# Performance work log

Hardware: AMD Instinct MI355X
Metric: run time of the kernel (lower is better)

## Reference

```python
import jax, jax.numpy as jnp
import numpy as np

DIM = 768
NUM_HEADS = 12
HEAD_DIM = DIM // NUM_HEADS
SCALE = HEAD_DIM ** -0.5


def setup_inputs() -> dict:
    key = jax.random.key(0)
    ks = jax.random.split(key, 4)
    x = jax.random.normal(ks[0], (8, 1024, DIM), dtype=jnp.float32)
    # nn.Linear stores weight as [out, in]; we keep that convention.
    w_qkv = jax.random.normal(ks[1], (3 * DIM, DIM), dtype=jnp.float32) * (DIM ** -0.5)
    w_proj = jax.random.normal(ks[2], (DIM, DIM), dtype=jnp.float32) * (DIM ** -0.5)
    b_proj = jax.random.normal(ks[3], (DIM,), dtype=jnp.float32) * 0.02
    return {"x": x, "w_qkv": w_qkv, "w_proj": w_proj, "b_proj": b_proj}


def reference(x, w_qkv, w_proj, b_proj):
    B, N, C = x.shape
    H, D = NUM_HEADS, HEAD_DIM
    # qkv: [B, N, 3C] -> [3, B, H, N, D]
    qkv = jnp.einsum('bnc,oc->bno', x, w_qkv)
    qkv = qkv.reshape(B, N, 3, H, D).transpose(2, 0, 3, 1, 4)
    q, k, v = qkv[0] * SCALE, qkv[1], qkv[2]
    # attention scores [B, H, N, N]
    attn = jnp.einsum('bhnd,bhmd->bhnm', q, k)
    attn = jax.nn.softmax(attn, axis=-1)
    # weighted values -> [B, N, C]
    out = jnp.einsum('bhnm,bhmd->bhnd', attn, v)
    out = out.transpose(0, 2, 1, 3).reshape(B, N, C)
    # output projection
    return jnp.einsum('bnc,oc->bno', out, w_proj) + b_proj
```

## Files before the change

### kernel.cpp

```cpp
#include <hip/hip_runtime.h>
#include <hip/hip_bf16.h>
#include <math.h>


typedef unsigned short u16;
typedef __attribute__((ext_vector_type(8))) short bf16x8;
typedef __attribute__((ext_vector_type(4))) float f32x4;
typedef __attribute__((ext_vector_type(4))) unsigned int u32x4;

#define MFMA_BF16(a, b, c) __builtin_amdgcn_mfma_f32_16x16x32_bf16((a), (b), (c), 0, 0, 0)

static __device__ __forceinline__ void gld_lds16(const void* g, void* l) {
  __builtin_amdgcn_global_load_lds(
      (__attribute__((address_space(1))) void*)(g),
      (__attribute__((address_space(3))) void*)(l), 16, 0, 0);
}

static __device__ __forceinline__ u16 f2bf(float f) {
  __hip_bfloat16 h = __float2bfloat16(f);
  return *(u16*)&h;
}

static __device__ __forceinline__ float fast_exp2(float x) {
#if __has_builtin(__builtin_amdgcn_exp2f)
  return __builtin_amdgcn_exp2f(x);
#else
  return exp2f(x);
#endif
}

static __device__ __forceinline__ void conv4(const float* src, u16* dst, int i) {
  const float4 v = *(const float4*)(src + i);
  float f0 = v.x, f1 = v.y, f2 = v.z, f3 = v.w;
  if (!isfinite(f0)) f0 = 0.f;
  if (!isfinite(f1)) f1 = 0.f;
  if (!isfinite(f2)) f2 = 0.f;
  if (!isfinite(f3)) f3 = 0.f;
  ushort4 o;
  o.x = f2bf(f0); o.y = f2bf(f1); o.z = f2bf(f2); o.w = f2bf(f3);
  *(ushort4*)(dst + i) = o;
}

__global__ __launch_bounds__(256) void convert3_kernel(
    const float* __restrict__ x,  u16* __restrict__ xb,
    const float* __restrict__ wq, u16* __restrict__ wqb,
    const float* __restrict__ wp, u16* __restrict__ wpb)
{
  const int blk = blockIdx.x;
  if (blk < 6144)      conv4(x,  xb,  (blk * 256 + threadIdx.x) * 4);
  else if (blk < 7872) conv4(wq, wqb, ((blk - 6144) * 256 + threadIdx.x) * 4);
  else                 conv4(wp, wpb, ((blk - 7872) * 256 + threadIdx.x) * 4);
}

__device__ __forceinline__ void gemm_tile_768(
    const u16* __restrict__ A, const u16* __restrict__ B,
    int m0, int n0, u16* ldsA, u16* ldsB, f32x4 acc[4][4])
{
  const int tid  = threadIdx.x;
  const int lane = tid & 63;
  const int wave = tid >> 6;
  const int quad = lane >> 4;
  const int l16  = lane & 15;
  const int wm = wave >> 1, wn = wave & 1;

  const u16* gA[4]; const u16* gB[4]; int ldsoff[4];
#pragma unroll
  for (int it = 0; it < 4; ++it) {
    const int c   = it * 256 + tid;
    const int row = c >> 3;
    const int cc  = (c & 7) ^ (row & 7);
    gA[it] = A + (size_t)(m0 + row) * 768 + cc * 8;
    gB[it] = B + (size_t)(n0 + row) * 768 + cc * 8;
    ldsoff[it] = (it * 256 + wave * 64) * 8;
  }

  for (int kt = 0; kt < 12; ++kt) {
    __syncthreads();
#pragma unroll
    for (int it = 0; it < 4; ++it) {
      gld_lds16(gA[it] + kt * 64, ldsA + ldsoff[it]);
      gld_lds16(gB[it] + kt * 64, ldsB + ldsoff[it]);
    }
    __syncthreads();
#pragma unroll
    for (int kc = 0; kc < 2; ++kc) {
      bf16x8 av[4], bv[4];
#pragma unroll
      for (int i = 0; i < 4; ++i) {
        const int rowA = wm * 64 + i * 16 + l16;
        av[i] = *(const bf16x8*)(ldsA + rowA * 64 + (((kc * 4 + quad) ^ (rowA & 7)) * 8));
        const int rowB = wn * 64 + i * 16 + l16;
        bv[i] = *(const bf16x8*)(ldsB + rowB * 64 + (((kc * 4 + quad) ^ (rowB & 7)) * 8));
      }
#pragma unroll
      for (int i = 0; i < 4; ++i)
#pragma unroll
        for (int j = 0; j < 4; ++j)
          acc[i][j] = MFMA_BF16(av[i], bv[j], acc[i][j]);
    }
  }
}


__global__ __launch_bounds__(256, 4) void qkv_gemm_kernel(
    const u16* __restrict__ X, const u16* __restrict__ W,
    u16* __restrict__ Qb, u16* __restrict__ Kb, u16* __restrict__ Vt)
{
  __shared__ alignas(16) u16 lds[2 * 128 * 64];
  u16* ldsA = lds;
  u16* ldsB = lds + 128 * 64;
  const int n0 = blockIdx.x * 128;
  const int m0 = blockIdx.y * 128;
  f32x4 acc[4][4];
  const f32x4 zero = {0.f, 0.f, 0.f, 0.f};
#pragma unroll
  for (int i = 0; i < 4; ++i)
#pragma unroll
    for (int j = 0; j < 4; ++j) acc[i][j] = zero;

  gemm_tile_768(X, W, m0, n0, ldsA, ldsB, acc);

  const int tid = threadIdx.x, lane = tid & 63, wave = tid >> 6;
  const int quad = lane >> 4, l16 = lane & 15;
  const int wm = wave >> 1, wn = wave & 1;

  const int which = blockIdx.x / 6;
  const bool isV = (which == 2);
  const float sc = (which == 0) ? 0.180336880f : 1.0f;
  u16* ep = lds;

  __syncthreads();
#pragma unroll
  for (int i = 0; i < 4; ++i)
#pragma unroll
    for (int j = 0; j < 4; ++j)
#pragma unroll
      for (int r = 0; r < 4; ++r) {
        const int m_l = wm * 64 + i * 16 + quad * 4 + r;
        const int o_l = wn * 64 + j * 16 + l16;
        const int row = isV ? o_l : m_l;
        const int col = isV ? m_l : o_l;
        const int ch  = col >> 3;
        const int chs = (ch & 8) | ((ch & 7) ^ (row & 7));
        ep[row * 128 + chs * 8 + (col & 7)] = f2bf(acc[i][j][r] * sc);
      }
  __syncthreads();

  const int row  = tid >> 1, half = tid & 1;
  const int b_   = m0 >> 10;
  const int nb   = m0 & 1023;
  const int oc0  = n0 - which * 768;
  u16* dst;
  if (!isV) {
    const int h = (oc0 >> 6) + half;
    dst = (which == 0 ? Qb : Kb) + (((size_t)(b_ * 12 + h)) * 1024 + nb + row) * 64;
  } else {
    const int h = (oc0 >> 6) + (row >> 6);
    const int d = row & 63;
    dst = Vt + (((size_t)(b_ * 12 + h)) * 64 + d) * 1024 + nb + half * 64;
  }
#pragma unroll
  for (int c = 0; c < 8; ++c) {
    const int chs = half * 8 + (c ^ (row & 7));
    *(u32x4*)(dst + c * 8) = *(const u32x4*)(ep + row * 128 + chs * 8);
  }
}

__global__ __launch_bounds__(256, 4) void proj_gemm_kernel(
    const u16* __restrict__ A, const u16* __restrict__ W,
    const float* __restrict__ bias, float* __restrict__ out)
{
  __shared__ alignas(16) u16 lds[2 * 128 * 64];
  u16* ldsA = lds;
  u16* ldsB = lds + 128 * 64;
  const int n0 = blockIdx.x * 128;
  const int m0 = blockIdx.y * 128;

  f32x4 acc[4][4];
  const f32x4 zero = {0.f, 0.f, 0.f, 0.f};
#pragma unroll
  for (int i = 0; i < 4; ++i)
#pragma unroll
    for (int j = 0; j < 4; ++j) acc[i][j] = zero;

  gemm_tile_768(A, W, m0, n0, ldsA, ldsB, acc);

  const int tid = threadIdx.x, lane = tid & 63, wave = tid >> 6;
  const int quad = lane >> 4, l16 = lane & 15;
  const int wm = wave >> 1, wn = wave & 1;

  float bv4[4];
#pragma unroll
  for (int j = 0; j < 4; ++j) bv4[j] = bias[n0 + wn * 64 + j * 16 + l16];

#pragma unroll
  for (int i = 0; i < 4; ++i)
#pragma unroll
    for (int j = 0; j < 4; ++j)
#pragma unroll
      for (int r = 0; r < 4; ++r) {
        const int m = m0 + wm * 64 + i * 16 + quad * 4 + r;
        out[(size_t)m * 768 + n0 + wn * 64 + j * 16 + l16] = acc[i][j][r] + bv4[j];
      }
}

__global__ __launch_bounds__(256, 3) void attn_kernel(
    const u16* __restrict__ Q, const u16* __restrict__ K,
    const u16* __restrict__ Vt, __hip_bfloat16* __restrict__ O)
{
  __shared__ alignas(16) u16 ldsK[128 * 64];
  __shared__ alignas(16) u16 ldsV[64 * 128];
  __shared__ alignas(16) u16 pbuf[4 * 32 * 72];
  const int bh = blockIdx.x;
  const int qb = blockIdx.y;
  const int tid = threadIdx.x;
  const int wave = tid >> 6, lane = tid & 63;
  const int quad = lane >> 4, l16 = lane & 15;
  u16* pw = pbuf + wave * (32 * 72);

  const int q0 = qb * 128 + wave * 32;
  const u16* Kbh = K  + (size_t)bh * (1024 * 64);
  const u16* Vbh = Vt + (size_t)bh * (64 * 1024);

  const u16* gK[4]; const u16* gV[4]; int loK[4], loV[4];
#pragma unroll
  for (int it = 0; it < 4; ++it) {
    const int c = it * 256 + tid;
    {
      const int row = c >> 3, cc = (c & 7) ^ (row & 7);
      gK[it] = Kbh + (size_t)row * 64 + cc * 8;
      loK[it] = (it * 256 + wave * 64) * 8;
    }
    {
      const int row = c >> 4, slot = c & 15;
      const int cc = (slot & 8) | ((slot & 7) ^ (row & 7));
      gV[it] = Vbh + (size_t)row * 1024 + cc * 8;
      loV[it] = (it * 256 + wave * 64) * 8;
    }
  }

  bf16x8 aQ0[2], aQ1[2];
#pragma unroll
  for (int s = 0; s < 2; ++s) {
    const u16* qp = Q + ((size_t)bh * 1024 + q0 + s * 16 + l16) * 64 + quad * 8;
    aQ0[s] = *(const bf16x8*)qp;
    aQ1[s] = *(const bf16x8*)(qp + 32);
  }

  f32x4 oacc[2][4];
  const f32x4 zero = {0.f, 0.f, 0.f, 0.f};
#pragma unroll
  for (int s = 0; s < 2; ++s)
#pragma unroll
    for (int db = 0; db < 4; ++db) oacc[s][db] = zero;
  float lacc[2] = {0.f, 0.f};

  for (int kt = 0; kt < 8; ++kt) {
    __syncthreads();
#pragma unroll
    for (int it = 0; it < 4; ++it) {
      gld_lds16(gK[it] + (size_t)kt * 128 * 64, ldsK + loK[it]);
      gld_lds16(gV[it] + kt * 128, ldsV + loV[it]);
    }
    __syncthreads();

#pragma unroll
    for (int ph = 0; ph < 2; ++ph) {
      bf16x8 kb0[4], kb1[4];
#pragma unroll
      for (int t = 0; t < 4; ++t) {
        const int row = ph * 64 + t * 16 + l16;
        kb0[t] = *(const bf16x8*)(ldsK + row * 64 + (((0 * 4 + quad) ^ (row & 7)) * 8));
        kb1[t] = *(const bf16x8*)(ldsK + row * 64 + (((1 * 4 + quad) ^ (row & 7)) * 8));
      }
      asm volatile("" ::: "memory");
#pragma unroll
      for (int s = 0; s < 2; ++s) {
#pragma unroll
        for (int t = 0; t < 4; ++t) {
          f32x4 z = zero;
          z = MFMA_BF16(kb0[t], aQ0[s], z);
          z = MFMA_BF16(kb1[t], aQ1[s], z);
          const float p0 = fast_exp2(z[0]);
          const float p1 = fast_exp2(z[1]);
          const float p2 = fast_exp2(z[2]);
          const float p3 = fast_exp2(z[3]);
          lacc[s] += (p0 + p1) + (p2 + p3);
          ushort4 pk;
          pk.x = f2bf(p0); pk.y = f2bf(p1); pk.z = f2bf(p2); pk.w = f2bf(p3);
          *(ushort4*)(pw + (s * 16 + l16) * 72 + t * 16 + quad * 4) = pk;
        }
      }
      asm volatile("" ::: "memory");
      bf16x8 pa0[2], pa1[2];
#pragma unroll
      for (int s = 0; s < 2; ++s) {
        const u16* pb = pw + (s * 16 + l16) * 72 + quad * 8;
        pa0[s] = *(const bf16x8*)pb;
        pa1[s] = *(const bf16x8*)(pb + 32);
      }
#pragma unroll
      for (int db = 0; db < 4; ++db) {
        const int d = db * 16 + l16;
        const bf16x8 v0 = *(const bf16x8*)(ldsV + d * 128 + (ph * 8 + ((0 * 4 + quad) ^ (d & 7))) * 8);
        const bf16x8 v1 = *(const bf16x8*)(ldsV + d * 128 + (ph * 8 + ((1 * 4 + quad) ^ (d & 7))) * 8);
#pragma unroll
        for (int s = 0; s < 2; ++s) {
          oacc[s][db] = MFMA_BF16(pa0[s], v0, oacc[s][db]);
          oacc[s][db] = MFMA_BF16(pa1[s], v1, oacc[s][db]);
        }
      }
    }
  }

  const int b = bh / 12, h = bh - (bh / 12) * 12;
  float linv[2];
#pragma unroll
  for (int s = 0; s < 2; ++s) {
    float l = lacc[s];
    l += __shfl_xor(l, 16);
    l += __shfl_xor(l, 32);
    linv[s] = 1.f / l;
  }
#pragma unroll
  for (int s = 0; s < 2; ++s) {
#pragma unroll
    for (int r = 0; r < 4; ++r) {
      const float inv = __shfl(linv[s], quad * 4 + r);
      const int n = q0 + s * 16 + quad * 4 + r;
      __hip_bfloat16* orow = O + ((size_t)b * 1024 + n) * 768 + h * 64;
#pragma unroll
      for (int db = 0; db < 4; ++db)
        orow[db * 16 + l16] = __float2bfloat16(oacc[s][db][r] * inv);
    }
  }
}

extern "C" void kernel_launch(void* const* d_in, const int* in_sizes, int n_in,
                              void* d_out, int out_size, void* d_ws, size_t ws_size,
                              hipStream_t stream) {
  const float* x      = (const float*)d_in[0];
  const float* w_qkv  = (const float*)d_in[1];
  const float* w_proj = (const float*)d_in[2];
  const float* b_proj = (const float*)d_in[3];
  float* out = (float*)d_out;

  char* ws = (char*)d_ws;
  const size_t SEG = (size_t)96 * 1024 * 64 * sizeof(u16);
  u16* xb   = (u16*)(ws + 0 * SEG);
  u16* Qb   = (u16*)(ws + 1 * SEG);
  u16* Kb   = (u16*)(ws + 2 * SEG);
  u16* AO   = (u16*)(ws + 3 * SEG);
  u16* Vt   = (u16*)(ws + 4 * SEG);
  u16* wqb  = (u16*)(ws + 5 * SEG);
  u16* wpb  = (u16*)(ws + 5 * SEG + 3538944);

  convert3_kernel<<<8448, 256, 0, stream>>>(x, xb, w_qkv, wqb, w_proj, wpb);
  qkv_gemm_kernel<<<dim3(18, 64), 256, 0, stream>>>(xb, wqb, Qb, Kb, Vt);
  attn_kernel    <<<dim3(96, 8), 256, 0, stream>>>(Qb, Kb, Vt, (__hip_bfloat16*)AO);
  proj_gemm_kernel<<<dim3(6, 64), 256, 0, stream>>>(AO, wpb, b_proj, out);
}
```

Before: 187.0 us.

## Register-prefetch next K/V tile during compute and raise MFMA wave priority

Replaces the direct global-to-LDS loads with a register-staged software pipeline. The next tile of K and V is loaded into registers while the current tile is computed, then written to LDS after the barrier, so global load latency overlaps with the MFMA work. It also wraps the MFMA sections with s_setprio so those waves get scheduling priority. The trade-off is extra VGPR pressure under launch_bounds(256,3) and explicit LDS store instructions in place of the async LDS load path.

```diff
diff --git a/kernel.cpp b/kernel.cpp
--- a/kernel.cpp
+++ b/kernel.cpp
@@ -222,20 +222,18 @@
   const u16* Kbh = K  + (size_t)bh * (1024 * 64);
   const u16* Vbh = Vt + (size_t)bh * (64 * 1024);
 
-  const u16* gK[4]; const u16* gV[4]; int loK[4], loV[4];
+  const u16* gK[4]; const u16* gV[4];
 #pragma unroll
   for (int it = 0; it < 4; ++it) {
     const int c = it * 256 + tid;
     {
       const int row = c >> 3, cc = (c & 7) ^ (row & 7);
       gK[it] = Kbh + (size_t)row * 64 + cc * 8;
-      loK[it] = (it * 256 + wave * 64) * 8;
     }
     {
       const int row = c >> 4, slot = c & 15;
       const int cc = (slot & 8) | ((slot & 7) ^ (row & 7));
       gV[it] = Vbh + (size_t)row * 1024 + cc * 8;
-      loV[it] = (it * 256 + wave * 64) * 8;
     }
   }
 
@@ -255,14 +253,33 @@
     for (int db = 0; db < 4; ++db) oacc[s][db] = zero;
   float lacc[2] = {0.f, 0.f};
 
+  u32x4 rK[4], rV[4];
+#pragma unroll
+  for (int it = 0; it < 4; ++it) {
+    rK[it] = *(const u32x4*)(gK[it]);
+    rV[it] = *(const u32x4*)(gV[it]);
+  }
+
   for (int kt = 0; kt < 8; ++kt) {
-    __syncthreads();
+    asm volatile("" ::: "memory");
+    __builtin_amdgcn_sched_barrier(0);
+    __builtin_amdgcn_s_barrier();
 #pragma unroll
     for (int it = 0; it < 4; ++it) {
-      gld_lds16(gK[it] + (size_t)kt * 128 * 64, ldsK + loK[it]);
-      gld_lds16(gV[it] + kt * 128, ldsV + loV[it]);
-    }
-    __syncthreads();
+      *(u32x4*)(ldsK + (size_t)(it * 256 + tid) * 8) = rK[it];
+      *(u32x4*)(ldsV + (size_t)(it * 256 + tid) * 8) = rV[it];
+    }
+    if (kt < 7) {
+#pragma unroll
+      for (int it = 0; it < 4; ++it) {
+        rK[it] = *(const u32x4*)(gK[it] + (size_t)(kt + 1) * 128 * 64);
+        rV[it] = *(const u32x4*)(gV[it] + (kt + 1) * 128);
+      }
+    }
+    asm volatile("s_waitcnt lgkmcnt(0)" ::: "memory");
+    __builtin_amdgcn_sched_barrier(0);
+    __builtin_amdgcn_s_barrier();
+    __builtin_amdgcn_sched_barrier(0);
 
 #pragma unroll
     for (int ph = 0; ph < 2; ++ph) {
@@ -279,8 +296,10 @@
 #pragma unroll
         for (int t = 0; t < 4; ++t) {
           f32x4 z = zero;
+          __builtin_amdgcn_s_setprio(1);
           z = MFMA_BF16(kb0[t], aQ0[s], z);
           z = MFMA_BF16(kb1[t], aQ1[s], z);
+          __builtin_amdgcn_s_setprio(0);
           const float p0 = fast_exp2(z[0]);
           const float p1 = fast_exp2(z[1]);
           const float p2 = fast_exp2(z[2]);
@@ -299,6 +318,7 @@
         pa0[s] = *(const bf16x8*)pb;
         pa1[s] = *(const bf16x8*)(pb + 32);
       }
+      __builtin_amdgcn_s_setprio(1);
 #pragma unroll
       for (int db = 0; db < 4; ++db) {
         const int d = db * 16 + l16;
@@ -310,6 +330,7 @@
           oacc[s][db] = MFMA_BF16(pa1[s], v1, oacc[s][db]);
         }
       }
+      __builtin_amdgcn_s_setprio(0);
     }
   }
 
```

Measured after the change: 224.3 us. 1.2x slower.

## Double-buffer K/V tiles in attention kernel to overlap loads with compute

Applied to the files above, without the earlier changes.

Replaces the single 128-key LDS tile with two 64-key buffers and prefetches the next tile via global_load_lds while computing on the current one. A single barrier per iteration replaces the previous two syncthreads. The aim is to hide global-to-LDS load latency behind MFMA and exp work. LDS footprint is unchanged, but iterations double and a vmcnt(0) wait is still taken at the top of each iteration.

```diff
diff --git a/kernel.cpp b/kernel.cpp
--- a/kernel.cpp
+++ b/kernel.cpp
@@ -208,8 +208,8 @@
     const u16* __restrict__ Q, const u16* __restrict__ K,
     const u16* __restrict__ Vt, __hip_bfloat16* __restrict__ O)
 {
-  __shared__ alignas(16) u16 ldsK[128 * 64];
-  __shared__ alignas(16) u16 ldsV[64 * 128];
+  __shared__ alignas(16) u16 ldsK[2 * 64 * 64];
+  __shared__ alignas(16) u16 ldsV[2 * 64 * 64];
   __shared__ alignas(16) u16 pbuf[4 * 32 * 72];
   const int bh = blockIdx.x;
   const int qb = blockIdx.y;
@@ -222,9 +222,9 @@
   const u16* Kbh = K  + (size_t)bh * (1024 * 64);
   const u16* Vbh = Vt + (size_t)bh * (64 * 1024);
 
-  const u16* gK[4]; const u16* gV[4]; int loK[4], loV[4];
-#pragma unroll
-  for (int it = 0; it < 4; ++it) {
+  const u16* gK[2]; const u16* gV[2]; int loK[2], loV[2];
+#pragma unroll
+  for (int it = 0; it < 2; ++it) {
     const int c = it * 256 + tid;
     {
       const int row = c >> 3, cc = (c & 7) ^ (row & 7);
@@ -232,8 +232,7 @@
       loK[it] = (it * 256 + wave * 64) * 8;
     }
     {
-      const int row = c >> 4, slot = c & 15;
-      const int cc = (slot & 8) | ((slot & 7) ^ (row & 7));
+      const int row = c >> 3, cc = (c & 7) ^ (row & 7);
       gV[it] = Vbh + (size_t)row * 1024 + cc * 8;
       loV[it] = (it * 256 + wave * 64) * 8;
     }
@@ -255,60 +254,70 @@
     for (int db = 0; db < 4; ++db) oacc[s][db] = zero;
   float lacc[2] = {0.f, 0.f};
 
-  for (int kt = 0; kt < 8; ++kt) {
-    __syncthreads();
-#pragma unroll
-    for (int it = 0; it < 4; ++it) {
-      gld_lds16(gK[it] + (size_t)kt * 128 * 64, ldsK + loK[it]);
-      gld_lds16(gV[it] + kt * 128, ldsV + loV[it]);
-    }
-    __syncthreads();
-
-#pragma unroll
-    for (int ph = 0; ph < 2; ++ph) {
-      bf16x8 kb0[4], kb1[4];
+#pragma unroll
+  for (int it = 0; it < 2; ++it) {
+    gld_lds16(gK[it], ldsK + loK[it]);
+    gld_lds16(gV[it], ldsV + loV[it]);
+  }
+
+#pragma unroll 2
+  for (int kt = 0; kt < 16; ++kt) {
+    const int cur = (kt & 1) * 4096;
+    asm volatile("s_waitcnt vmcnt(0)" ::: "memory");
+    __builtin_amdgcn_sched_barrier(0);
+    __builtin_amdgcn_s_barrier();
+    __builtin_amdgcn_sched_barrier(0);
+    if (kt < 15) {
+      const int nxt = ((kt + 1) & 1) * 4096;
+#pragma unroll
+      for (int it = 0; it < 2; ++it) {
+        gld_lds16(gK[it] + (size_t)(kt + 1) * (64 * 64), ldsK + nxt + loK[it]);
+        gld_lds16(gV[it] + (kt + 1) * 64, ldsV + nxt + loV[it]);
+      }
+    }
+
+    bf16x8 kb0[4], kb1[4];
+#pragma unroll
+    for (int t = 0; t < 4; ++t) {
+      const int row = t * 16 + l16;
+      kb0[t] = *(const bf16x8*)(ldsK + cur + row * 64 + (((0 * 4 + quad) ^ (row & 7)) * 8));
+      kb1[t] = *(const bf16x8*)(ldsK + cur + row * 64 + (((1 * 4 + quad) ^ (row & 7)) * 8));
+    }
+    asm volatile("" ::: "memory");
+#pragma unroll
+    for (int s = 0; s < 2; ++s) {
 #pragma unroll
       for (int t = 0; t < 4; ++t) {
-        const int row = ph * 64 + t * 16 + l16;
-        kb0[t] = *(const bf16x8*)(ldsK + row * 64 + (((0 * 4 + quad) ^ (row & 7)) * 8));
-        kb1[t] = *(const bf16x8*)(ldsK + row * 64 + (((1 * 4 + quad) ^ (row & 7)) * 8));
-      }
-      asm volatile("" ::: "memory");
+        f32x4 z = zero;
+        z = MFMA_BF16(kb0[t], aQ0[s], z);
+        z = MFMA_BF16(kb1[t], aQ1[s], z);
+        const float p0 = fast_exp2(z[0]);
+        const float p1 = fast_exp2(z[1]);
+        const float p2 = fast_exp2(z[2]);
+        const float p3 = fast_exp2(z[3]);
+        lacc[s] += (p0 + p1) + (p2 + p3);
+        ushort4 pk;
+        pk.x = f2bf(p0); pk.y = f2bf(p1); pk.z = f2bf(p2); pk.w = f2bf(p3);
+        *(ushort4*)(pw + (s * 16 + l16) * 72 + t * 16 + quad * 4) = pk;
+      }
+    }
+    asm volatile("" ::: "memory");
+    bf16x8 pa0[2], pa1[2];
+#pragma unroll
+    for (int s = 0; s < 2; ++s) {
+      const u16* pb = pw + (s * 16 + l16) * 72 + quad * 8;
+      pa0[s] = *(const bf16x8*)pb;
+      pa1[s] = *(const bf16x8*)(pb + 32);
+    }
+#pragma unroll
+    for (int db = 0; db < 4; ++db) {
+      const int d = db * 16 + l16;
+      const bf16x8 v0 = *(const bf16x8*)(ldsV + cur + d * 64 + (((0 * 4 + quad) ^ (d & 7))) * 8);
+      const bf16x8 v1 = *(const bf16x8*)(ldsV + cur + d * 64 + (((1 * 4 + quad) ^ (d & 7))) * 8);
 #pragma unroll
       for (int s = 0; s < 2; ++s) {
-#pragma unroll
-        for (int t = 0; t < 4; ++t) {
-          f32x4 z = zero;
-          z = MFMA_BF16(kb0[t], aQ0[s], z);
-          z = MFMA_BF16(kb1[t], aQ1[s], z);
-          const float p0 = fast_exp2(z[0]);
-          const float p1 = fast_exp2(z[1]);
-          const float p2 = fast_exp2(z[2]);
-          const float p3 = fast_exp2(z[3]);
-          lacc[s] += (p0 + p1) + (p2 + p3);
-          ushort4 pk;
-          pk.x = f2bf(p0); pk.y = f2bf(p1); pk.z = f2bf(p2); pk.w = f2bf(p3);
-          *(ushort4*)(pw + (s * 16 + l16) * 72 + t * 16 + quad * 4) = pk;
-        }
-      }
-      asm volatile("" ::: "memory");
-      bf16x8 pa0[2], pa1[2];
-#pragma unroll
-      for (int s = 0; s < 2; ++s) {
-        const u16* pb = pw + (s * 16 + l16) * 72 + quad * 8;
-        pa0[s] = *(const bf16x8*)pb;
-        pa1[s] = *(const bf16x8*)(pb + 32);
-      }
-#pragma unroll
-      for (int db = 0; db < 4; ++db) {
-        const int d = db * 16 + l16;
-        const bf16x8 v0 = *(const bf16x8*)(ldsV + d * 128 + (ph * 8 + ((0 * 4 + quad) ^ (d & 7))) * 8);
-        const bf16x8 v1 = *(const bf16x8*)(ldsV + d * 128 + (ph * 8 + ((1 * 4 + quad) ^ (d & 7))) * 8);
-#pragma unroll
-        for (int s = 0; s < 2; ++s) {
-          oacc[s][db] = MFMA_BF16(pa0[s], v0, oacc[s][db]);
-          oacc[s][db] = MFMA_BF16(pa1[s], v1, oacc[s][db]);
-        }
+        oacc[s][db] = MFMA_BF16(pa0[s], v0, oacc[s][db]);
+        oacc[s][db] = MFMA_BF16(pa1[s], v1, oacc[s][db]);
       }
     }
   }
```

After: 185.9 us. Within noise of the previous version (-0.6%).
